# Performance work log

Hardware: AMD Instinct MI355X
Metric: run time of the kernel (lower is better)

The kernel has to match this reference:

```python
import jax, jax.numpy as jnp
import numpy as np

ALPHA, BETA, GAMMA, DELTA = 0.3, 0.3, 0.2, 0.2
BK, BW = 3, 3.0
EPS = 1e-7


def _bce_with_logits(x, y):
    # numerically stable: max(x,0) - x*y + log(1+exp(-|x|)); pos_weight=1.0
    return jnp.maximum(x, 0.0) - x * y + jnp.log1p(jnp.exp(-jnp.abs(x)))


def _lovasz_hinge_flat(x, y):
    # x, y: (N,) flattened logits / binary labels for one image
    signs = 2.0 * y - 1.0
    errors = 1.0 - x * signs
    perm = jnp.argsort(-errors)            # descending sort permutation
    errors_sorted = errors[perm]
    gt_sorted = y[perm]
    gts = gt_sorted.sum()
    intersection = gts - jnp.cumsum(gt_sorted)
    union = gts + jnp.cumsum(1.0 - gt_sorted)
    jaccard = 1.0 - intersection / union
    jaccard = jnp.concatenate([jaccard[:1], jaccard[1:] - jaccard[:-1]])
    return jnp.dot(jax.nn.relu(errors_sorted), jaccard)


def setup_inputs() -> dict:
    key = jax.random.key(0)
    k1, k2 = jax.random.split(key)
    logits = jax.random.normal(k1, (32, 1, 512, 512), dtype=jnp.float32)
    # binary ground-truth mask (0/1 floats)
    targets = jnp.round(jax.random.uniform(k2, (32, 1, 512, 512), dtype=jnp.float32))
    return {"logits": logits, "targets": targets}


def reference(logits, targets):
    # --- BCE term (pos_weight = 1.0) ---
    bce_elem = _bce_with_logits(logits, targets)
    bce = bce_elem.mean()

    # --- Dice term ---
    probs = jax.nn.sigmoid(logits)
    num = 2.0 * (probs * targets).sum(axis=(2, 3))
    den = (probs + targets).sum(axis=(2, 3)) + EPS
    dice = 1.0 - (num / den).mean()

    # --- Boundary-weighted BCE term (weights computed under no_grad) ---
    kernel = jnp.ones((1, 1, BK, BK), logits.dtype) / (BK * BK)
    smooth = jax.lax.conv_general_dilated(
        targets, kernel, window_strides=(1, 1), padding='SAME',
        dimension_numbers=('NCHW', 'OIHW', 'NCHW'))
    edges = ((smooth > 0.01) & (smooth < 0.99)).astype(logits.dtype)
    weights = jax.lax.stop_gradient(1.0 + edges * (BW - 1.0))
    boundary = (bce_elem * weights).mean()

    # --- Lovasz hinge, per image then averaged ---
    B = logits.shape[0]
    lov = jax.vmap(_lovasz_hinge_flat)(
        logits.reshape(B, -1), targets.reshape(B, -1)).mean()

    return ALPHA * bce + BETA * dice + GAMMA * boundary + DELTA * lov
```

## Files before the change

kernel.cpp:

```cpp
#include <hip/hip_runtime.h>
#include <hip/hip_bf16.h>


#define NB      32
#define HH      512
#define WW      512
#define HW      (HH*WW)
#define NTOT    (NB*HW)
#define K_BINS  1024
#define INV_H   128.0f
#define BIN_W   (1.0f/128.0f)

struct Ws {
    unsigned cnt[NB*K_BINS];
    float    sy[NB];
    float    spy[NB];
    float    Pim[NB];
    float    bce_sum;
    float    bceE_sum;
    float    lov_sum;
    unsigned blkdone[NB];
    unsigned imgdone;
};

__device__ __forceinline__ float dpp_from_lower(float v) {
    const int r = __builtin_amdgcn_update_dpp(0, __float_as_int(v), 0x130, 0xF, 0xF, false);
    return __int_as_float(r);
}
__device__ __forceinline__ float dpp_from_upper(float v) {
    const int r = __builtin_amdgcn_update_dpp(0, __float_as_int(v), 0x138, 0xF, 0xF, false);
    return __int_as_float(r);
}
__device__ __forceinline__ float bcast_lane(float v, int lane) {
    return __int_as_float(__builtin_amdgcn_readlane(__float_as_int(v), lane));
}

__device__ __forceinline__ int process_elem(float x, float y, float wsum,
                                            float& bce_s, float& bceE_s, float& sy_s,
                                            float& spy_s, float& P_s) {
    const float ax = fabsf(x);
    const float t  = __expf(-ax);
    const float bce = fmaxf(x, 0.f) - x * y + __logf(1.f + t);
    const float inv = __builtin_amdgcn_rcpf(1.f + t);
    const float s = (x >= 0.f) ? inv : t * inv;
    const bool edge = (wsum > 0.5f) && (wsum < 8.5f);

    bce_s  += bce;
    bceE_s += edge ? bce : 0.f;
    sy_s   += s * y;
    spy_s  += s + y;
    P_s    += y;

    const float e = 1.f - x * (2.f * y - 1.f);
    if (e > 0.f) {
        int b = (int)(e * INV_H);
        if (b > K_BINS - 1) b = K_BINS - 1;
        return (y > 0.5f) ? (b | 0x10000) : b;
    }
    return -1;
}

__global__ __launch_bounds__(256, 2) void kernelA(const float* __restrict__ logits,
                                                  const float* __restrict__ targets,
                                                  Ws* __restrict__ ws,
                                                  float* __restrict__ out) {
    __shared__ unsigned s_cnt[K_BINS];
    __shared__ float    red[4][5];
    __shared__ unsigned sc_a[256];
    __shared__ unsigned sc_p[256];
    __shared__ double   dred[4];
    __shared__ unsigned s_flag, s_flag2;

    const int tid  = threadIdx.x;
    const int lane = tid & 63;
    const int wave = tid >> 6;
    for (int i = tid; i < K_BINS; i += 256) s_cnt[i] = 0u;
    __syncthreads();

    const int img   = blockIdx.x >> 4;
    const int strip = ((blockIdx.x & 15) << 2) | wave;
    const int r0    = strip * 8;

    const float4* __restrict__ tg4 = (const float4*)(targets + img * HW);
    const float4* __restrict__ lg4 = (const float4*)(logits  + img * HW);
    const int cA = lane;
    const int cB = 64 + lane;

#define HADD(expr) do { \
        const int _r = (expr); \
        if (_r >= 0) { \
            const unsigned _inc = (_r & 0x10000) ? 0x10001u : 1u; \
            (void)__hip_atomic_fetch_add(&s_cnt[_r & 0xFFFF], _inc, \
                                         __ATOMIC_RELAXED, __HIP_MEMORY_SCOPE_WORKGROUP); \
        } \
    } while (0)

    float4 T[5][2]; float fT[5];
    float4 X[3][2];

#pragma unroll
    for (int s = 0; s < 5; ++s) {
        const int rr = r0 - 1 + s;
        const int rc = rr < 0 ? 0 : (rr > 511 ? 511 : rr);
        fT[s] = (rr >= 0 && rr < 512) ? 1.f : 0.f;
        T[s][0] = tg4[rc * 128 + cA];
        T[s][1] = tg4[rc * 128 + cB];
    }
#pragma unroll
    for (int s = 0; s < 3; ++s) {
        const int rr = r0 + s;
        X[s][0] = lg4[rr * 128 + cA];
        X[s][1] = lg4[rr * 128 + cB];
    }

    float bce_s = 0.f, bceE_s = 0.f, sy_s = 0.f, spy_s = 0.f, P_s = 0.f;

#pragma unroll
    for (int j = 0; j < 8; ++j) {
        const int ia = j % 5, ib = (j + 1) % 5, ic = (j + 2) % 5;
        const int xs = j % 3;
        const float fa = fT[ia], fc = fT[ic];

        float4 csA, csB;
        csA.x = fmaf(T[ia][0].x, fa, fmaf(T[ic][0].x, fc, T[ib][0].x));
        csA.y = fmaf(T[ia][0].y, fa, fmaf(T[ic][0].y, fc, T[ib][0].y));
        csA.z = fmaf(T[ia][0].z, fa, fmaf(T[ic][0].z, fc, T[ib][0].z));
        csA.w = fmaf(T[ia][0].w, fa, fmaf(T[ic][0].w, fc, T[ib][0].w));
        csB.x = fmaf(T[ia][1].x, fa, fmaf(T[ic][1].x, fc, T[ib][1].x));
        csB.y = fmaf(T[ia][1].y, fa, fmaf(T[ic][1].y, fc, T[ib][1].y));
        csB.z = fmaf(T[ia][1].z, fa, fmaf(T[ic][1].z, fc, T[ib][1].z));
        csB.w = fmaf(T[ia][1].w, fa, fmaf(T[ic][1].w, fc, T[ib][1].w));

        const float upA  = dpp_from_lower(csA.w);
        const float dnA  = dpp_from_upper(csA.x);
        const float upB  = dpp_from_lower(csB.w);
        const float dnB  = dpp_from_upper(csB.x);
        const float bc0  = bcast_lane(csB.x, 0);
        const float bc63 = bcast_lane(csA.w, 63);
        const float LA = (lane == 0)  ? 0.f  : upA;
        const float RA = (lane == 63) ? bc0  : dnA;
        const float LB = (lane == 0)  ? bc63 : upB;
        const float RB = (lane == 63) ? 0.f  : dnB;

        HADD(process_elem(X[xs][0].x, T[ib][0].x, LA + csA.x + csA.y,    bce_s, bceE_s, sy_s, spy_s, P_s));
        HADD(process_elem(X[xs][0].y, T[ib][0].y, csA.x + csA.y + csA.z, bce_s, bceE_s, sy_s, spy_s, P_s));
        HADD(process_elem(X[xs][0].z, T[ib][0].z, csA.y + csA.z + csA.w, bce_s, bceE_s, sy_s, spy_s, P_s));
        HADD(process_elem(X[xs][0].w, T[ib][0].w, csA.z + csA.w + RA,    bce_s, bceE_s, sy_s, spy_s, P_s));
        HADD(process_elem(X[xs][1].x, T[ib][1].x, LB + csB.x + csB.y,    bce_s, bceE_s, sy_s, spy_s, P_s));
        HADD(process_elem(X[xs][1].y, T[ib][1].y, csB.x + csB.y + csB.z, bce_s, bceE_s, sy_s, spy_s, P_s));
        HADD(process_elem(X[xs][1].z, T[ib][1].z, csB.y + csB.z + csB.w, bce_s, bceE_s, sy_s, spy_s, P_s));
        HADD(process_elem(X[xs][1].w, T[ib][1].w, csB.z + csB.w + RB,    bce_s, bceE_s, sy_s, spy_s, P_s));

        if (j < 5) {
            const int rr = r0 + j + 4;
            const int rc = rr > 511 ? 511 : rr;
            fT[ia] = (rr < 512) ? 1.f : 0.f;
            T[ia][0] = tg4[rc * 128 + cA];
            T[ia][1] = tg4[rc * 128 + cB];
            const int rx = r0 + j + 3;
            X[xs][0] = lg4[rx * 128 + cA];
            X[xs][1] = lg4[rx * 128 + cB];
        }
    }
#undef HADD
    __syncthreads();

    unsigned* g_c = ws->cnt + img * K_BINS;
    for (int i = tid; i < K_BINS; i += 256) {
        const unsigned cpk = s_cnt[i];
        if (cpk) atomicAdd(&g_c[i], cpk);
    }

    for (int off = 32; off; off >>= 1) {
        bce_s  += __shfl_down(bce_s, off);
        bceE_s += __shfl_down(bceE_s, off);
        sy_s   += __shfl_down(sy_s, off);
        spy_s  += __shfl_down(spy_s, off);
        P_s    += __shfl_down(P_s, off);
    }
    if (lane == 0) {
        red[wave][0] = bce_s; red[wave][1] = bceE_s; red[wave][2] = sy_s;
        red[wave][3] = spy_s; red[wave][4] = P_s;
    }
    __syncthreads();
    if (tid == 0) {
        float a = 0.f, b = 0.f, c2 = 0.f, d = 0.f, e2 = 0.f;
        for (int w = 0; w < 4; ++w) {
            a += red[w][0]; b += red[w][1]; c2 += red[w][2];
            d += red[w][3]; e2 += red[w][4];
        }
        atomicAdd(&ws->bce_sum, a);
        atomicAdd(&ws->bceE_sum, b);
        atomicAdd(&ws->sy[img], c2);
        atomicAdd(&ws->spy[img], d);
        atomicAdd(&ws->Pim[img], e2);
        __threadfence();
        const unsigned d16 = atomicAdd(&ws->blkdone[img], 1u);
        s_flag = (d16 == 15u) ? 1u : 0u;
    }
    __syncthreads();

    if (s_flag) {
        unsigned* cn = ws->cnt + img * K_BINS;

        unsigned la[4], lp[4];
        float    me[4];
        unsigned tot_a = 0, tot_p = 0;
#pragma unroll
        for (int j = 0; j < 4; ++j) {
            const int k = K_BINS - 1 - (tid * 4 + j);
            const unsigned cpk = atomicAdd(&cn[k], 0u);
            la[j] = cpk & 0xFFFFu; lp[j] = cpk >> 16;
            me[j] = ((float)k + 0.5f) * BIN_W;
            tot_a += la[j]; tot_p += lp[j];
        }

        sc_a[tid] = tot_a; sc_p[tid] = tot_p;
        __syncthreads();
        for (int off = 1; off < 256; off <<= 1) {
            unsigned va = (tid >= off) ? sc_a[tid - off] : 0u;
            unsigned vp = (tid >= off) ? sc_p[tid - off] : 0u;
            __syncthreads();
            sc_a[tid] += va; sc_p[tid] += vp;
            __syncthreads();
        }
        const unsigned excl_a = sc_a[tid] - tot_a;
        const unsigned excl_p = sc_p[tid] - tot_p;

        const double P = (double)atomicAdd(&ws->Pim[img], 0.f);
        double run_a = (double)excl_a, run_p = (double)excl_p;
        double contrib = 0.0;
#pragma unroll
        for (int j = 0; j < 4; ++j) {
            const double m = (double)la[j];
            const double p = (double)lp[j];
            if (la[j]) {
                const double u = P + (run_a + 0.5 * m) - (run_p + 0.5 * p);
                const double c = run_p + 0.5 * p;
                contrib += (double)(lp[j] * me[j]) / u;
                const double den = u * (u - 1.0);
                if (den > 0.0)
                    contrib += (double)((la[j] - lp[j]) * me[j]) * (P - c) / den;
            }
            run_a += m; run_p += p;
        }

        for (int off = 32; off; off >>= 1) contrib += __shfl_down(contrib, off);
        if (lane == 0) dred[wave] = contrib;
        __syncthreads();
        if (tid == 0) {
            const double tot = dred[0] + dred[1] + dred[2] + dred[3];
            atomicAdd(&ws->lov_sum, (float)tot);
            __threadfence();
            const unsigned d32 = atomicAdd(&ws->imgdone, 1u);
            s_flag2 = (d32 == (unsigned)(NB - 1)) ? 1u : 0u;
        }
        __syncthreads();

        if (s_flag2 && wave == 0) {
            float dsum = 0.f;
            if (lane < NB) {
                const float syv  = atomicAdd(&ws->sy[lane], 0.f);
                const float spyv = atomicAdd(&ws->spy[lane], 0.f);
                dsum = 2.f * syv / (spyv + 1e-7f);
            }
            for (int off = 32; off; off >>= 1) dsum += __shfl_down(dsum, off);
            if (lane == 0) {
                const float bsum = atomicAdd(&ws->bce_sum, 0.f);
                const float besm = atomicAdd(&ws->bceE_sum, 0.f);
                const float lsum = atomicAdd(&ws->lov_sum, 0.f);
                const float invN = 1.f / (float)NTOT;
                const float bce      = bsum * invN;
                const float boundary = (bsum + 2.f * besm) * invN;
                const float dice     = 1.f - dsum / (float)NB;
                const float lov      = lsum / (float)NB;
                out[0] = 0.3f * bce + 0.3f * dice + 0.2f * boundary + 0.2f * lov;
            }
        }
    }
}

extern "C" void kernel_launch(void* const* d_in, const int* in_sizes, int n_in,
                              void* d_out, int out_size, void* d_ws, size_t ws_size,
                              hipStream_t stream) {
    const float* logits  = (const float*)d_in[0];
    const float* targets = (const float*)d_in[1];
    float* out = (float*)d_out;
    Ws* ws = (Ws*)d_ws;

    (void)hipMemsetAsync(d_ws, 0, sizeof(Ws), stream);
    kernelA<<<NB * 16, 256, 0, stream>>>(logits, targets, ws, out);
}
```

Before: 118.4 us.

## Stage target and logit tiles in LDS via direct global-to-LDS loads

Each block now covers 16 rows of one image, so there are 32 blocks per image instead of 16. It first loads 18 target rows (with halo) and 16 logit rows straight into LDS using global_load_lds, then each wave streams 4 rows from shared memory. This removes the redundant halo reloads per wave-strip and frees registers from the rotating row buffers. In exchange it uses about 68KB of LDS per block, which limits occupancy, and it loses the overlap between loads and compute because all data is fetched before a barrier.

```diff
diff --git a/kernel.cpp b/kernel.cpp
--- a/kernel.cpp
+++ b/kernel.cpp
@@ -10,6 +10,9 @@
 #define K_BINS  1024
 #define INV_H   128.0f
 #define BIN_W   (1.0f/128.0f)
+#define BPI     32
+#define LROWS   16
+#define TROWS   18
 
 struct Ws {
     unsigned cnt[NB*K_BINS];
@@ -23,6 +26,12 @@
     unsigned imgdone;
 };
 
+__device__ __forceinline__ void gload_lds16(const float* __restrict__ g, float* l) {
+    __builtin_amdgcn_global_load_lds(
+        (const __attribute__((address_space(1))) void*)g,
+        (__attribute__((address_space(3))) void*)l, 16, 0, 0);
+}
+
 __device__ __forceinline__ float dpp_from_lower(float v) {
     const int r = __builtin_amdgcn_update_dpp(0, __float_as_int(v), 0x130, 0xF, 0xF, false);
     return __int_as_float(r);
@@ -64,6 +73,8 @@
                                                   const float* __restrict__ targets,
                                                   Ws* __restrict__ ws,
                                                   float* __restrict__ out) {
+    __shared__ float    s_tgt[TROWS * WW];
+    __shared__ float    s_lgt[LROWS * WW];
     __shared__ unsigned s_cnt[K_BINS];
     __shared__ float    red[4][5];
     __shared__ unsigned sc_a[256];
@@ -74,17 +85,33 @@
     const int tid  = threadIdx.x;
     const int lane = tid & 63;
     const int wave = tid >> 6;
+
     for (int i = tid; i < K_BINS; i += 256) s_cnt[i] = 0u;
+
+    const int img = blockIdx.x >> 5;
+    const int blk = blockIdx.x & 31;
+    const int r0  = blk * 16;
+
+    const float* __restrict__ tg = targets + img * HW;
+    const float* __restrict__ lg = logits  + img * HW;
+
+#pragma unroll
+    for (int k = 0; k < 9; ++k) {
+        const int c     = wave * 9 + k;
+        const int rslot = c >> 1;
+        int gr = r0 - 1 + rslot;
+        gr = gr < 0 ? 0 : (gr > 511 ? 511 : gr);
+        const int h = (c & 1) * 256;
+        gload_lds16(tg + gr * WW + h + lane * 4, s_tgt + rslot * WW + h + lane * 4);
+    }
+#pragma unroll
+    for (int k = 0; k < 8; ++k) {
+        const int c     = wave * 8 + k;
+        const int rslot = c >> 1;
+        const int h     = (c & 1) * 256;
+        gload_lds16(lg + (r0 + rslot) * WW + h + lane * 4, s_lgt + rslot * WW + h + lane * 4);
+    }
     __syncthreads();
-
-    const int img   = blockIdx.x >> 4;
-    const int strip = ((blockIdx.x & 15) << 2) | wave;
-    const int r0    = strip * 8;
-
-    const float4* __restrict__ tg4 = (const float4*)(targets + img * HW);
-    const float4* __restrict__ lg4 = (const float4*)(logits  + img * HW);
-    const int cA = lane;
-    const int cB = 64 + lane;
 
 #define HADD(expr) do { \
         const int _r = (expr); \
@@ -95,41 +122,38 @@
         } \
     } while (0)
 
-    float4 T[5][2]; float fT[5];
-    float4 X[3][2];
-
-#pragma unroll
-    for (int s = 0; s < 5; ++s) {
-        const int rr = r0 - 1 + s;
-        const int rc = rr < 0 ? 0 : (rr > 511 ? 511 : rr);
-        fT[s] = (rr >= 0 && rr < 512) ? 1.f : 0.f;
-        T[s][0] = tg4[rc * 128 + cA];
-        T[s][1] = tg4[rc * 128 + cB];
-    }
-#pragma unroll
-    for (int s = 0; s < 3; ++s) {
-        const int rr = r0 + s;
-        X[s][0] = lg4[rr * 128 + cA];
-        X[s][1] = lg4[rr * 128 + cB];
-    }
+    const int cA = 4 * lane;
+    const int cB = 256 + 4 * lane;
+
+    const int s0 = wave * 4;
 
     float bce_s = 0.f, bceE_s = 0.f, sy_s = 0.f, spy_s = 0.f, P_s = 0.f;
 
-#pragma unroll
-    for (int j = 0; j < 8; ++j) {
-        const int ia = j % 5, ib = (j + 1) % 5, ic = (j + 2) % 5;
-        const int xs = j % 3;
-        const float fa = fT[ia], fc = fT[ic];
+    float4 Tt0 = *(const float4*)&s_tgt[(s0    ) * WW + cA];
+    float4 Tt1 = *(const float4*)&s_tgt[(s0    ) * WW + cB];
+    float4 Tm0 = *(const float4*)&s_tgt[(s0 + 1) * WW + cA];
+    float4 Tm1 = *(const float4*)&s_tgt[(s0 + 1) * WW + cB];
+
+#pragma unroll
+    for (int q = 0; q < 4; ++q) {
+        const float4 Tb0 = *(const float4*)&s_tgt[(s0 + q + 2) * WW + cA];
+        const float4 Tb1 = *(const float4*)&s_tgt[(s0 + q + 2) * WW + cB];
+        const float4 X0  = *(const float4*)&s_lgt[(s0 + q) * WW + cA];
+        const float4 X1  = *(const float4*)&s_lgt[(s0 + q) * WW + cB];
+
+        const int   grow = r0 + s0 + q;
+        const float fa = (grow > 0)   ? 1.f : 0.f;
+        const float fc = (grow < 511) ? 1.f : 0.f;
 
         float4 csA, csB;
-        csA.x = fmaf(T[ia][0].x, fa, fmaf(T[ic][0].x, fc, T[ib][0].x));
-        csA.y = fmaf(T[ia][0].y, fa, fmaf(T[ic][0].y, fc, T[ib][0].y));
-        csA.z = fmaf(T[ia][0].z, fa, fmaf(T[ic][0].z, fc, T[ib][0].z));
-        csA.w = fmaf(T[ia][0].w, fa, fmaf(T[ic][0].w, fc, T[ib][0].w));
-        csB.x = fmaf(T[ia][1].x, fa, fmaf(T[ic][1].x, fc, T[ib][1].x));
-        csB.y = fmaf(T[ia][1].y, fa, fmaf(T[ic][1].y, fc, T[ib][1].y));
-        csB.z = fmaf(T[ia][1].z, fa, fmaf(T[ic][1].z, fc, T[ib][1].z));
-        csB.w = fmaf(T[ia][1].w, fa, fmaf(T[ic][1].w, fc, T[ib][1].w));
+        csA.x = fmaf(Tt0.x, fa, fmaf(Tb0.x, fc, Tm0.x));
+        csA.y = fmaf(Tt0.y, fa, fmaf(Tb0.y, fc, Tm0.y));
+        csA.z = fmaf(Tt0.z, fa, fmaf(Tb0.z, fc, Tm0.z));
+        csA.w = fmaf(Tt0.w, fa, fmaf(Tb0.w, fc, Tm0.w));
+        csB.x = fmaf(Tt1.x, fa, fmaf(Tb1.x, fc, Tm1.x));
+        csB.y = fmaf(Tt1.y, fa, fmaf(Tb1.y, fc, Tm1.y));
+        csB.z = fmaf(Tt1.z, fa, fmaf(Tb1.z, fc, Tm1.z));
+        csB.w = fmaf(Tt1.w, fa, fmaf(Tb1.w, fc, Tm1.w));
 
         const float upA  = dpp_from_lower(csA.w);
         const float dnA  = dpp_from_upper(csA.x);
@@ -142,25 +166,16 @@
         const float LB = (lane == 0)  ? bc63 : upB;
         const float RB = (lane == 63) ? 0.f  : dnB;
 
-        HADD(process_elem(X[xs][0].x, T[ib][0].x, LA + csA.x + csA.y,    bce_s, bceE_s, sy_s, spy_s, P_s));
-        HADD(process_elem(X[xs][0].y, T[ib][0].y, csA.x + csA.y + csA.z, bce_s, bceE_s, sy_s, spy_s, P_s));
-        HADD(process_elem(X[xs][0].z, T[ib][0].z, csA.y + csA.z + csA.w, bce_s, bceE_s, sy_s, spy_s, P_s));
-        HADD(process_elem(X[xs][0].w, T[ib][0].w, csA.z + csA.w + RA,    bce_s, bceE_s, sy_s, spy_s, P_s));
-        HADD(process_elem(X[xs][1].x, T[ib][1].x, LB + csB.x + csB.y,    bce_s, bceE_s, sy_s, spy_s, P_s));
-        HADD(process_elem(X[xs][1].y, T[ib][1].y, csB.x + csB.y + csB.z, bce_s, bceE_s, sy_s, spy_s, P_s));
-        HADD(process_elem(X[xs][1].z, T[ib][1].z, csB.y + csB.z + csB.w, bce_s, bceE_s, sy_s, spy_s, P_s));
-        HADD(process_elem(X[xs][1].w, T[ib][1].w, csB.z + csB.w + RB,    bce_s, bceE_s, sy_s, spy_s, P_s));
-
-        if (j < 5) {
-            const int rr = r0 + j + 4;
-            const int rc = rr > 511 ? 511 : rr;
-            fT[ia] = (rr < 512) ? 1.f : 0.f;
-            T[ia][0] = tg4[rc * 128 + cA];
-            T[ia][1] = tg4[rc * 128 + cB];
-            const int rx = r0 + j + 3;
-            X[xs][0] = lg4[rx * 128 + cA];
-            X[xs][1] = lg4[rx * 128 + cB];
-        }
+        HADD(process_elem(X0.x, Tm0.x, LA + csA.x + csA.y,    bce_s, bceE_s, sy_s, spy_s, P_s));
+        HADD(process_elem(X0.y, Tm0.y, csA.x + csA.y + csA.z, bce_s, bceE_s, sy_s, spy_s, P_s));
+        HADD(process_elem(X0.z, Tm0.z, csA.y + csA.z + csA.w, bce_s, bceE_s, sy_s, spy_s, P_s));
+        HADD(process_elem(X0.w, Tm0.w, csA.z + csA.w + RA,    bce_s, bceE_s, sy_s, spy_s, P_s));
+        HADD(process_elem(X1.x, Tm1.x, LB + csB.x + csB.y,    bce_s, bceE_s, sy_s, spy_s, P_s));
+        HADD(process_elem(X1.y, Tm1.y, csB.x + csB.y + csB.z, bce_s, bceE_s, sy_s, spy_s, P_s));
+        HADD(process_elem(X1.z, Tm1.z, csB.y + csB.z + csB.w, bce_s, bceE_s, sy_s, spy_s, P_s));
+        HADD(process_elem(X1.w, Tm1.w, csB.z + csB.w + RB,    bce_s, bceE_s, sy_s, spy_s, P_s));
+
+        Tt0 = Tm0; Tt1 = Tm1; Tm0 = Tb0; Tm1 = Tb1;
     }
 #undef HADD
     __syncthreads();
@@ -195,8 +210,8 @@
         atomicAdd(&ws->spy[img], d);
         atomicAdd(&ws->Pim[img], e2);
         __threadfence();
-        const unsigned d16 = atomicAdd(&ws->blkdone[img], 1u);
-        s_flag = (d16 == 15u) ? 1u : 0u;
+        const unsigned dcnt = atomicAdd(&ws->blkdone[img], 1u);
+        s_flag = (dcnt == (unsigned)(BPI - 1)) ? 1u : 0u;
     }
     __syncthreads();
 
@@ -289,5 +304,5 @@
     Ws* ws = (Ws*)d_ws;
 
     (void)hipMemsetAsync(d_ws, 0, sizeof(Ws), stream);
-    kernelA<<<NB * 16, 256, 0, stream>>>(logits, targets, ws, out);
-}
+    kernelA<<<NB * BPI, 256, 0, stream>>>(logits, targets, ws, out);
+}
```

After: 141.1 us. 1.19x slower.
